# Kernel tuning notes

Measured on AMD Instinct MI355X. Metric: run time of the kernel, lower is better.

## Reference

```python
import jax, jax.numpy as jnp
import numpy as np

REF_CHANNEL = 0
DIAG_EPS = 1e-7   # diag_loading coefficient
TIK_EPS = 1e-8    # additive eps in diagonal loading / trace denominator
MASK_EPS = 1e-15  # PSD mask-normalization eps


def _psd(spec, mask):
    # spec: (b, c, f, t) complex; mask: (b, f, t) real
    # PSD module: normalize mask over time, weight outer products, sum over t.
    m = mask / (mask.sum(axis=-1, keepdims=True) + MASK_EPS)
    return jnp.einsum('bcft,beft,bft->bfce', spec, spec.conj(), m.astype(spec.dtype))


def setup_inputs() -> dict:
    key = jax.random.key(0)
    k1, k2, k3, k4 = jax.random.split(key, 4)
    B, C, F, T = 4, 6, 257, 2000
    return {
        'spec_real': jax.random.normal(k1, (B, C, F, T), dtype=jnp.float32),
        'spec_imag': jax.random.normal(k2, (B, C, F, T), dtype=jnp.float32),
        'mask_s': jax.random.uniform(k3, (B, F, T), dtype=jnp.float32),
        'mask_n': jax.random.uniform(k4, (B, F, T), dtype=jnp.float32),
    }


def reference(spec_real, spec_imag, mask_s, mask_n):
    spec = spec_real + 1j * spec_imag                     # (b, c, f, t) complex64
    C = spec.shape[1]

    psd_s = _psd(spec, mask_s)                            # (b, f, c, c)
    psd_n = _psd(spec, mask_n)                            # (b, f, c, c)

    # Diagonal loading (Tikhonov regularization) of the noise PSD.
    tr_n = jnp.einsum('bfcc->bf', psd_n).real
    epsilon = jax.lax.stop_gradient(tr_n * DIAG_EPS + TIK_EPS)   # torch uses no_grad here
    psd_n = psd_n + epsilon[..., None, None] * jnp.eye(C, dtype=spec.dtype)

    # ref_channel solution: w = (psd_n^-1 psd_s) / trace(psd_n^-1 psd_s) @ u
    numerator = jnp.linalg.solve(psd_n, psd_s)            # (b, f, c, c)
    tr = jnp.einsum('bfcc->bf', numerator)
    ws = numerator / (tr[..., None, None] + TIK_EPS)
    w = ws[..., :, REF_CHANNEL]                           # one-hot u selects column -> (b, f, c)

    # enhanced = w^H Y
    enh = jnp.einsum('bfc,bcft->bft', w.conj(), spec)     # (b, f, t) complex
    return jnp.stack([enh.real, enh.imag], axis=-1)       # (b, f, t, 2) float32
```

## Files before the change

### kernel.cpp

```cpp
#include <hip/hip_runtime.h>

#define NB 4
#define NC 6
#define NF 257
#define NT 2000
#define NG (NB * NF)
#define NPAIR 15
#define NACC 74
#define BLK 256
#define CS  (NF * NT)
#define CS4 (CS / 4)
#define NP4G (NT / 4)
#define HALF4 (NP4G / 2)

typedef float nfloat4 __attribute__((ext_vector_type(4)));

__device__ __forceinline__ void psd_acc_pos(
    const float4* __restrict__ s4r, const float4* __restrict__ s4i,
    const float4* __restrict__ m4s, const float4* __restrict__ m4n,
    int p, float (&acc)[NACC])
{
    constexpr int PC[NPAIR] = {0,0,0,0,0,1,1,1,1,2,2,2,3,3,4};
    constexpr int PE[NPAIR] = {1,2,3,4,5,2,3,4,5,3,4,5,4,5,5};

    float wms[4], wmn[4], rr[NC][4], ii[NC][4];
    {
        const float4 t0 = m4s[p];
        wms[0] = t0.x; wms[1] = t0.y; wms[2] = t0.z; wms[3] = t0.w;
        const float4 t1 = m4n[p];
        wmn[0] = t1.x; wmn[1] = t1.y; wmn[2] = t1.z; wmn[3] = t1.w;
    }
    #pragma unroll
    for (int c = 0; c < NC; c++) {
        const float4 tr = s4r[c * CS4 + p];
        rr[c][0] = tr.x; rr[c][1] = tr.y; rr[c][2] = tr.z; rr[c][3] = tr.w;
        const float4 ti = s4i[c * CS4 + p];
        ii[c][0] = ti.x; ii[c][1] = ti.y; ii[c][2] = ti.z; ii[c][3] = ti.w;
    }
    #pragma unroll
    for (int k = 0; k < 4; k++) { acc[72] += wms[k]; acc[73] += wmn[k]; }
    #pragma unroll
    for (int c = 0; c < NC; c++) {
        #pragma unroll
        for (int k = 0; k < 4; k++) {
            const float d = rr[c][k] * rr[c][k] + ii[c][k] * ii[c][k];
            acc[c]     += d * wms[k];
            acc[6 + c] += d * wmn[k];
        }
    }
    #pragma unroll
    for (int q = 0; q < NPAIR; q++) {
        const int c = PC[q], e = PE[q];
        #pragma unroll
        for (int k = 0; k < 4; k++) {
            const float cr = rr[c][k] * rr[e][k] + ii[c][k] * ii[e][k];
            const float ci = ii[c][k] * rr[e][k] - rr[c][k] * ii[e][k];
            acc[12 + 4 * q + 0] += cr * wms[k];
            acc[12 + 4 * q + 1] += ci * wms[k];
            acc[12 + 4 * q + 2] += cr * wmn[k];
            acc[12 + 4 * q + 3] += ci * wmn[k];
        }
    }
}

__global__ __launch_bounds__(BLK) void psd_kernel(
    const float* __restrict__ sr, const float* __restrict__ si,
    const float* __restrict__ ms, const float* __restrict__ mn,
    float* __restrict__ wsp)
{
    const int g  = blockIdx.x;
    const int b  = g / NF;
    const int f  = g - b * NF;
    const int sbase = b * NC * CS + f * NT;
    const int mbase = g * NT;

    const float4* s4r = (const float4*)(sr + sbase);
    const float4* s4i = (const float4*)(si + sbase);
    const float4* m4s = (const float4*)(ms + mbase);
    const float4* m4n = (const float4*)(mn + mbase);

    float acc[NACC];
    #pragma unroll
    for (int i = 0; i < NACC; i++) acc[i] = 0.f;

    const int p = threadIdx.x;
    if (p < HALF4) {
        psd_acc_pos(s4r, s4i, m4s, m4n, p, acc);
        psd_acc_pos(s4r, s4i, m4s, m4n, p + HALF4, acc);
    }

    #pragma unroll
    for (int i = 0; i < NACC; i++) {
        float v = acc[i];
        v += __shfl_down(v, 32);
        v += __shfl_down(v, 16);
        v += __shfl_down(v, 8);
        acc[i] = v;
    }

    __shared__ float red[32][NACC];
    const int wid  = threadIdx.x >> 6;
    const int lane = threadIdx.x & 63;
    if (lane < 8) {
        #pragma unroll
        for (int i = 0; i < NACC; i++) red[wid * 8 + lane][i] = acc[i];
    }
    __syncthreads();

    if (threadIdx.x < NACC) {
        float s = 0.f;
        #pragma unroll
        for (int r = 0; r < 32; r++) s += red[r][threadIdx.x];
        wsp[g * NACC + threadIdx.x] = s;
    }
}

__global__ __launch_bounds__(64, 1) void solve_kernel(
    const float* __restrict__ wsp, float* __restrict__ wsw)
{
    const int gid = blockIdx.x * 64 + threadIdx.x;
    if (gid >= NG) return;

    constexpr int PC[NPAIR] = {0,0,0,0,0,1,1,1,1,2,2,2,3,3,4};
    constexpr int PE[NPAIR] = {1,2,3,4,5,2,3,4,5,3,4,5,4,5,5};
    constexpr int QIDX[NC][NC] = {
        {-1, 0, 1, 2, 3, 4},
        {-1,-1, 5, 6, 7, 8},
        {-1,-1,-1, 9,10,11},
        {-1,-1,-1,-1,12,13},
        {-1,-1,-1,-1,-1,14},
        {-1,-1,-1,-1,-1,-1}};

    float fin[NACC];
    #pragma unroll
    for (int i = 0; i < NACC; i++) fin[i] = wsp[gid * NACC + i];

    const float invS = 1.f / (fin[72] + 1e-15f);
    const float invN = 1.f / (fin[73] + 1e-15f);

    float Ar[NC][NC], Ai[NC][NC];
    #pragma unroll
    for (int c = 0; c < NC; c++) { Ar[c][c] = fin[6 + c] * invN; Ai[c][c] = 0.f; }
    #pragma unroll
    for (int q = 0; q < NPAIR; q++) {
        const int c = PC[q], e = PE[q];
        const float nre = fin[12 + 4 * q + 2] * invN;
        const float nim = fin[12 + 4 * q + 3] * invN;
        Ar[c][e] = nre;  Ai[c][e] = nim;
        Ar[e][c] = nre;  Ai[e][c] = -nim;
    }
    {
        float trn = 0.f;
        #pragma unroll
        for (int c = 0; c < NC; c++) trn += Ar[c][c];
        const float eps = trn * 1e-7f + 1e-8f;
        #pragma unroll
        for (int c = 0; c < NC; c++) Ar[c][c] += eps;
    }

    #pragma unroll
    for (int k = 0; k < NC; k++) {
        const float dr = Ar[k][k], di = Ai[k][k];
        const float idn = 1.f / (dr * dr + di * di);
        const float pr = dr * idn, pi = -di * idn;
        #pragma unroll
        for (int i = k + 1; i < NC; i++) {
            const float lr = Ar[i][k] * pr - Ai[i][k] * pi;
            const float li = Ar[i][k] * pi + Ai[i][k] * pr;
            Ar[i][k] = lr; Ai[i][k] = li;
            #pragma unroll
            for (int j = k + 1; j < NC; j++) {
                Ar[i][j] -= lr * Ar[k][j] - li * Ai[k][j];
                Ai[i][j] -= lr * Ai[k][j] + li * Ar[k][j];
            }
        }
    }

    float trr = 1e-8f, tri = 0.f;
    float w0r[NC], w0i[NC];
    #pragma unroll
    for (int j = 0; j < NC; j++) {
        float xr[NC], xi[NC];
        #pragma unroll
        for (int i = 0; i < NC; i++) {
            if (i == j)      { xr[i] = fin[j] * invS;                      xi[i] = 0.f; }
            else if (i < j)  { const int q = QIDX[i][j];
                               xr[i] = fin[12 + 4 * q] * invS;  xi[i] =  fin[13 + 4 * q] * invS; }
            else             { const int q = QIDX[j][i];
                               xr[i] = fin[12 + 4 * q] * invS;  xi[i] = -fin[13 + 4 * q] * invS; }
        }
        #pragma unroll
        for (int i = 1; i < NC; i++) {
            #pragma unroll
            for (int k = 0; k < NC - 1; k++) if (k < i) {
                xr[i] -= Ar[i][k] * xr[k] - Ai[i][k] * xi[k];
                xi[i] -= Ar[i][k] * xi[k] + Ai[i][k] * xr[k];
            }
        }
        #pragma unroll
        for (int i = NC - 1; i >= 0; i--) {
            #pragma unroll
            for (int k = 0; k < NC; k++) if (k > i) {
                xr[i] -= Ar[i][k] * xr[k] - Ai[i][k] * xi[k];
                xi[i] -= Ar[i][k] * xi[k] + Ai[i][k] * xr[k];
            }
            const float dr = Ar[i][i], di = Ai[i][i];
            const float idn = 1.f / (dr * dr + di * di);
            const float pr = dr * idn, pi = -di * idn;
            const float tr0 = xr[i] * pr - xi[i] * pi;
            xi[i] = xr[i] * pi + xi[i] * pr;
            xr[i] = tr0;
        }
        trr += xr[j]; tri += xi[j];
        if (j == 0) {
            #pragma unroll
            for (int i = 0; i < NC; i++) { w0r[i] = xr[i]; w0i[i] = xi[i]; }
        }
    }

    const float idn = 1.f / (trr * trr + tri * tri);
    #pragma unroll
    for (int c = 0; c < NC; c++) {
        const float wre = (w0r[c] * trr + w0i[c] * tri) * idn;
        const float wim = (w0i[c] * trr - w0r[c] * tri) * idn;
        wsw[gid * 12 + c]     = wre;
        wsw[gid * 12 + 6 + c] = -wim;
    }
}

__global__ __launch_bounds__(BLK) void apply_kernel(
    const float* __restrict__ sr, const float* __restrict__ si,
    const float* __restrict__ wsw, float* __restrict__ out)
{
    const int bx = blockIdx.x;
    const int g  = bx >> 1;
    const int b  = g / NF;
    const int f  = g - b * NF;
    const int tb = (bx & 1) * (NT / 2);
    const int sbase = b * NC * CS + f * NT + tb;

    const float4* s4r = (const float4*)(sr + sbase);
    const float4* s4i = (const float4*)(si + sbase);

    float wr[NC], wi[NC];
    #pragma unroll
    for (int c = 0; c < NC; c++) {
        wr[c] = wsw[g * 12 + c];
        wi[c] = wsw[g * 12 + 6 + c];
    }

    nfloat4* o4 = (nfloat4*)(out + 2 * (g * NT + tb));

    const int p = threadIdx.x;
    if (p < HALF4) {
        float rr[NC][4], ii[NC][4];
        #pragma unroll
        for (int c = 0; c < NC; c++) {
            const float4 tr = s4r[c * CS4 + p];
            rr[c][0] = tr.x; rr[c][1] = tr.y; rr[c][2] = tr.z; rr[c][3] = tr.w;
            const float4 ti = s4i[c * CS4 + p];
            ii[c][0] = ti.x; ii[c][1] = ti.y; ii[c][2] = ti.z; ii[c][3] = ti.w;
        }
        float er[4], ei[4];
        #pragma unroll
        for (int k = 0; k < 4; k++) {
            float a = 0.f, bb = 0.f;
            #pragma unroll
            for (int c = 0; c < NC; c++) {
                a  += wr[c] * rr[c][k] - wi[c] * ii[c][k];
                bb += wr[c] * ii[c][k] + wi[c] * rr[c][k];
            }
            er[k] = a; ei[k] = bb;
        }
        nfloat4 o0 = {er[0], ei[0], er[1], ei[1]};
        nfloat4 o1 = {er[2], ei[2], er[3], ei[3]};
        __builtin_nontemporal_store(o0, &o4[2 * p]);
        __builtin_nontemporal_store(o1, &o4[2 * p + 1]);
    }
}

extern "C" void kernel_launch(void* const* d_in, const int* in_sizes, int n_in,
                              void* d_out, int out_size, void* d_ws, size_t ws_size,
                              hipStream_t stream) {
    const float* sr = (const float*)d_in[0];
    const float* si = (const float*)d_in[1];
    const float* ms = (const float*)d_in[2];
    const float* mn = (const float*)d_in[3];
    float* out = (float*)d_out;

    float* wsp = (float*)d_ws;
    float* wsw = wsp + NG * NACC;

    psd_kernel<<<NG, BLK, 0, stream>>>(sr, si, ms, mn, wsp);
    solve_kernel<<<(NG + 63) / 64, 64, 0, stream>>>(wsp, wsw);
    apply_kernel<<<NG * 2, BLK, 0, stream>>>(sr, si, wsw, out);
}
```

Baseline: 176.0 us.

## Split PSD accumulation across two time-chunk blocks and use DPP reductions

```diff
diff --git a/kernel.cpp b/kernel.cpp
--- a/kernel.cpp
+++ b/kernel.cpp
@@ -7,72 +7,36 @@
 #define NG (NB * NF)
 #define NPAIR 15
 #define NACC 74
+#define NCHUNK 2
+#define TCH (NT / NCHUNK)
+#define NP4 (TCH / 4)
 #define BLK 256
 #define CS  (NF * NT)
 #define CS4 (CS / 4)
-#define NP4G (NT / 4)
-#define HALF4 (NP4G / 2)
 
 typedef float nfloat4 __attribute__((ext_vector_type(4)));
 
-__device__ __forceinline__ void psd_acc_pos(
-    const float4* __restrict__ s4r, const float4* __restrict__ s4i,
-    const float4* __restrict__ m4s, const float4* __restrict__ m4n,
-    int p, float (&acc)[NACC])
-{
-    constexpr int PC[NPAIR] = {0,0,0,0,0,1,1,1,1,2,2,2,3,3,4};
-    constexpr int PE[NPAIR] = {1,2,3,4,5,2,3,4,5,3,4,5,4,5,5};
-
-    float wms[4], wmn[4], rr[NC][4], ii[NC][4];
-    {
-        const float4 t0 = m4s[p];
-        wms[0] = t0.x; wms[1] = t0.y; wms[2] = t0.z; wms[3] = t0.w;
-        const float4 t1 = m4n[p];
-        wmn[0] = t1.x; wmn[1] = t1.y; wmn[2] = t1.z; wmn[3] = t1.w;
-    }
-    #pragma unroll
-    for (int c = 0; c < NC; c++) {
-        const float4 tr = s4r[c * CS4 + p];
-        rr[c][0] = tr.x; rr[c][1] = tr.y; rr[c][2] = tr.z; rr[c][3] = tr.w;
-        const float4 ti = s4i[c * CS4 + p];
-        ii[c][0] = ti.x; ii[c][1] = ti.y; ii[c][2] = ti.z; ii[c][3] = ti.w;
-    }
-    #pragma unroll
-    for (int k = 0; k < 4; k++) { acc[72] += wms[k]; acc[73] += wmn[k]; }
-    #pragma unroll
-    for (int c = 0; c < NC; c++) {
-        #pragma unroll
-        for (int k = 0; k < 4; k++) {
-            const float d = rr[c][k] * rr[c][k] + ii[c][k] * ii[c][k];
-            acc[c]     += d * wms[k];
-            acc[6 + c] += d * wmn[k];
-        }
-    }
-    #pragma unroll
-    for (int q = 0; q < NPAIR; q++) {
-        const int c = PC[q], e = PE[q];
-        #pragma unroll
-        for (int k = 0; k < 4; k++) {
-            const float cr = rr[c][k] * rr[e][k] + ii[c][k] * ii[e][k];
-            const float ci = ii[c][k] * rr[e][k] - rr[c][k] * ii[e][k];
-            acc[12 + 4 * q + 0] += cr * wms[k];
-            acc[12 + 4 * q + 1] += ci * wms[k];
-            acc[12 + 4 * q + 2] += cr * wmn[k];
-            acc[12 + 4 * q + 3] += ci * wmn[k];
-        }
-    }
-}
-
-__global__ __launch_bounds__(BLK) void psd_kernel(
+template<int CTRL>
+__device__ __forceinline__ float dpp_add(float v) {
+    int s = __builtin_amdgcn_update_dpp(0, __builtin_bit_cast(int, v), CTRL, 0xF, 0xF, true);
+    return v + __builtin_bit_cast(float, s);
+}
+
+__global__ __launch_bounds__(BLK, 4) void psd_kernel(
     const float* __restrict__ sr, const float* __restrict__ si,
     const float* __restrict__ ms, const float* __restrict__ mn,
     float* __restrict__ wsp)
 {
-    const int g  = blockIdx.x;
+    constexpr int PC[NPAIR] = {0,0,0,0,0,1,1,1,1,2,2,2,3,3,4};
+    constexpr int PE[NPAIR] = {1,2,3,4,5,2,3,4,5,3,4,5,4,5,5};
+
+    const int bx = blockIdx.x;
+    const int g  = bx >> 1;
     const int b  = g / NF;
     const int f  = g - b * NF;
-    const int sbase = b * NC * CS + f * NT;
-    const int mbase = g * NT;
+    const int tb = (bx & 1) * TCH;
+    const int sbase = b * NC * CS + f * NT + tb;
+    const int mbase = g * NT + tb;
 
     const float4* s4r = (const float4*)(sr + sbase);
     const float4* s4i = (const float4*)(si + sbase);
@@ -83,27 +47,68 @@
     #pragma unroll
     for (int i = 0; i < NACC; i++) acc[i] = 0.f;
 
-    const int p = threadIdx.x;
-    if (p < HALF4) {
-        psd_acc_pos(s4r, s4i, m4s, m4n, p, acc);
-        psd_acc_pos(s4r, s4i, m4s, m4n, p + HALF4, acc);
+    const bool act = threadIdx.x < NP4;
+    const int  p   = act ? threadIdx.x : 0;
+    {
+        float wms[4], wmn[4], rr[NC][4], ii[NC][4];
+        {
+            const float4 t0 = m4s[p];
+            wms[0] = t0.x; wms[1] = t0.y; wms[2] = t0.z; wms[3] = t0.w;
+            const float4 t1 = m4n[p];
+            wmn[0] = t1.x; wmn[1] = t1.y; wmn[2] = t1.z; wmn[3] = t1.w;
+        }
+        #pragma unroll
+        for (int c = 0; c < NC; c++) {
+            const float4 tr = s4r[c * CS4 + p];
+            rr[c][0] = tr.x; rr[c][1] = tr.y; rr[c][2] = tr.z; rr[c][3] = tr.w;
+            const float4 ti = s4i[c * CS4 + p];
+            ii[c][0] = ti.x; ii[c][1] = ti.y; ii[c][2] = ti.z; ii[c][3] = ti.w;
+        }
+        if (!act) {
+            #pragma unroll
+            for (int k = 0; k < 4; k++) { wms[k] = 0.f; wmn[k] = 0.f; }
+        }
+        #pragma unroll
+        for (int k = 0; k < 4; k++) { acc[72] += wms[k]; acc[73] += wmn[k]; }
+        #pragma unroll
+        for (int c = 0; c < NC; c++) {
+            #pragma unroll
+            for (int k = 0; k < 4; k++) {
+                const float d = rr[c][k] * rr[c][k] + ii[c][k] * ii[c][k];
+                acc[c]     += d * wms[k];
+                acc[6 + c] += d * wmn[k];
+            }
+        }
+        #pragma unroll
+        for (int q = 0; q < NPAIR; q++) {
+            const int c = PC[q], e = PE[q];
+            #pragma unroll
+            for (int k = 0; k < 4; k++) {
+                const float cr = rr[c][k] * rr[e][k] + ii[c][k] * ii[e][k];
+                const float ci = ii[c][k] * rr[e][k] - rr[c][k] * ii[e][k];
+                acc[12 + 4 * q + 0] += cr * wms[k];
+                acc[12 + 4 * q + 1] += ci * wms[k];
+                acc[12 + 4 * q + 2] += cr * wmn[k];
+                acc[12 + 4 * q + 3] += ci * wmn[k];
+            }
+        }
     }
 
     #pragma unroll
     for (int i = 0; i < NACC; i++) {
         float v = acc[i];
-        v += __shfl_down(v, 32);
-        v += __shfl_down(v, 16);
-        v += __shfl_down(v, 8);
+        v = dpp_add<0x118>(v);
+        v = dpp_add<0x114>(v);
+        v = dpp_add<0x112>(v);
         acc[i] = v;
     }
 
     __shared__ float red[32][NACC];
-    const int wid  = threadIdx.x >> 6;
-    const int lane = threadIdx.x & 63;
-    if (lane < 8) {
-        #pragma unroll
-        for (int i = 0; i < NACC; i++) red[wid * 8 + lane][i] = acc[i];
+    const int lane16 = threadIdx.x & 15;
+    const int ridx   = ((threadIdx.x >> 4) << 1) | (lane16 & 1);
+    if (lane16 >= 14) {
+        #pragma unroll
+        for (int i = 0; i < NACC; i++) red[ridx][i] = acc[i];
     }
     __syncthreads();
 
@@ -111,7 +116,7 @@
         float s = 0.f;
         #pragma unroll
         for (int r = 0; r < 32; r++) s += red[r][threadIdx.x];
-        wsp[g * NACC + threadIdx.x] = s;
+        wsp[bx * NACC + threadIdx.x] = s;
     }
 }
 
@@ -131,9 +136,11 @@
         {-1,-1,-1,-1,-1,14},
         {-1,-1,-1,-1,-1,-1}};
 
+    const float* p0 = wsp + (2 * gid) * NACC;
+    const float* p1 = p0 + NACC;
     float fin[NACC];
     #pragma unroll
-    for (int i = 0; i < NACC; i++) fin[i] = wsp[gid * NACC + i];
+    for (int i = 0; i < NACC; i++) fin[i] = p0[i] + p1[i];
 
     const float invS = 1.f / (fin[72] + 1e-15f);
     const float invN = 1.f / (fin[73] + 1e-15f);
@@ -236,7 +243,7 @@
     const int g  = bx >> 1;
     const int b  = g / NF;
     const int f  = g - b * NF;
-    const int tb = (bx & 1) * (NT / 2);
+    const int tb = (bx & 1) * TCH;
     const int sbase = b * NC * CS + f * NT + tb;
 
     const float4* s4r = (const float4*)(sr + sbase);
@@ -252,7 +259,7 @@
     nfloat4* o4 = (nfloat4*)(out + 2 * (g * NT + tb));
 
     const int p = threadIdx.x;
-    if (p < HALF4) {
+    if (p < NP4) {
         float rr[NC][4], ii[NC][4];
         #pragma unroll
         for (int c = 0; c < NC; c++) {
@@ -289,9 +296,9 @@
     float* out = (float*)d_out;
 
     float* wsp = (float*)d_ws;
-    float* wsw = wsp + NG * NACC;
-
-    psd_kernel<<<NG, BLK, 0, stream>>>(sr, si, ms, mn, wsp);
+    float* wsw = wsp + NG * NCHUNK * NACC;
+
+    psd_kernel<<<NG * NCHUNK, BLK, 0, stream>>>(sr, si, ms, mn, wsp);
     solve_kernel<<<(NG + 63) / 64, 64, 0, stream>>>(wsp, wsw);
-    apply_kernel<<<NG * 2, BLK, 0, stream>>>(sr, si, wsw, out);
-}
+    apply_kernel<<<NG * NCHUNK, BLK, 0, stream>>>(sr, si, wsw, out);
+}
```

New measurement: 201.2 us. 14.3% more time.
